# Performance work log

Measured on AMD Instinct MI355X. Metric: run time of the kernel, lower is better.

Reference implementation:

```python
import jax, jax.numpy as jnp
import numpy as np

B, S, A = 4096, 512, 64  # batch, state_dim, n_actions
H1, H2 = 1024, 512       # hidden_dims
EPS = 1e-8


def setup_inputs() -> dict:
    key = jax.random.key(0)
    ks = jax.random.split(key, 7)
    return {
        "states": jax.random.normal(ks[0], (B, S), dtype=jnp.float32),
        "W1": jax.random.normal(ks[1], (H1, S + A), dtype=jnp.float32) * 0.05,
        "b1": jax.random.normal(ks[2], (H1,), dtype=jnp.float32) * 0.01,
        "W2": jax.random.normal(ks[3], (H2, H1), dtype=jnp.float32) * 0.05,
        "b2": jax.random.normal(ks[4], (H2,), dtype=jnp.float32) * 0.01,
        "Wq": jax.random.normal(ks[5], (1, H2), dtype=jnp.float32) * 0.05,
        "bq": jax.random.normal(ks[6], (1,), dtype=jnp.float32) * 0.01,
    }


def _ff_layer(h, W, b):
    # L2-normalize over feature dim (torch dim=1 for 2D input), then linear + ReLU
    hn = h / (jnp.linalg.norm(h, axis=-1, keepdims=True) + EPS)
    return jax.nn.relu(jnp.einsum("abi,oi->abo", hn, W) + b)


def reference(states, W1, b1, W2, b2, Wq, bq):
    # Vectorized form of q_values: loop over actions becomes a leading axis a.
    # x_in[a, b] = concat(states[b], one_hot(a))  (overlay_type='standard')
    onehot = jnp.eye(A, dtype=states.dtype)                         # [A, A]
    x = jnp.concatenate(
        [jnp.broadcast_to(states[None], (A, B, S)),
         jnp.broadcast_to(onehot[:, None, :], (A, B, A))], axis=-1)  # [A, B, S+A]
    h = _ff_layer(x, W1, b1)   # [A, B, H1]
    h = _ff_layer(h, W2, b2)   # [A, B, H2]
    q = jnp.einsum("abh,oh->abo", h, Wq)[..., 0] + bq[0]            # [A, B]
    return q.T                                                       # [B, A]
```

## Files before the change

### kernel.cpp

```cpp
#include <hip/hip_runtime.h>
#include <stdint.h>

#define NB 4096
#define NS 512
#define NA 64
#define NH1 1024
#define NH2 512

typedef __attribute__((ext_vector_type(8))) short bf16x8;
typedef __attribute__((ext_vector_type(4))) float f32x4;

__device__ __forceinline__ unsigned short f2bf(float f) {
    union { float f; unsigned u; } v; v.f = f;
    return (unsigned short)((v.u + 0x8000u) >> 16);
}
__device__ __forceinline__ float bf2f(unsigned short h) {
    union { float f; unsigned u; } v; v.u = ((unsigned)h) << 16;
    return v.f;
}
__device__ __forceinline__ float bflo(unsigned u) {
    union { unsigned u; float f; } v; v.u = u << 16; return v.f;
}
__device__ __forceinline__ float bfhi(unsigned u) {
    union { unsigned u; float f; } v; v.u = u & 0xFFFF0000u; return v.f;
}
__device__ __forceinline__ unsigned packtrunc(float lo, float hi) {
    union { float f; unsigned u; } a, b; a.f = lo; b.f = hi;
    return __builtin_amdgcn_perm(b.u, a.u, 0x07060302u);
}
__device__ __forceinline__ void split2(float x, unsigned short& h, unsigned short& l) {
    unsigned short hh = f2bf(x);
    h = hh;
    l = f2bf(x - bf2f(hh));
}

__global__ void knorm(const float* __restrict__ S, float* __restrict__ nb) {
    int b = blockIdx.x; int l = threadIdx.x;
    const float* row = S + b * NS;
    float s = 0.f;
    for (int k = l; k < NS; k += 64) { float v = row[k]; s = fmaf(v, v, s); }
    for (int off = 32; off; off >>= 1) s += __shfl_down(s, off, 64);
    if (l == 0) nb[b] = sqrtf(s + 1.0f) + 1e-8f;
}

__global__ void kprep(const float* __restrict__ W1, const float* __restrict__ W2,
                      unsigned short* __restrict__ W2f, unsigned short* __restrict__ caT2,
                      unsigned short* __restrict__ W1hf, unsigned short* __restrict__ W1lf) {
    int i = blockIdx.x * 256 + threadIdx.x;
    if (i < 524288) {
        int j = i & 7; int l = (i >> 3) & 63; int c = (i >> 9) & 31; int kc = i >> 14;
        int n = c * 16 + (l >> 2);
        int g = (l & 3) ^ ((n >> 1) & 3);
        int k = kc * 32 + g * 8 + j;
        W2f[i] = f2bf(W2[(size_t)n * NH1 + k]);
    } else if (i < 589824) {
        int j2 = i - 524288;
        int kk = j2 & 31; int a_loc = (j2 >> 5) & 15;
        int kc = (j2 >> 9) & 31; int att = j2 >> 14;
        int o = kc * 32 + kk;
        caT2[j2] = f2bf(W1[(size_t)o * 576 + 512 + att * 16 + a_loc]);
    } else {
        int i2 = i - 589824;
        int kk = i2 & 31; int n = (i2 >> 5) & 1023; int kc = i2 >> 15;
        float x = W1[(size_t)n * 576 + kc * 32 + kk];
        unsigned short h, l;
        split2(x, h, l);
        W1hf[i2] = h;
        W1lf[i2] = l;
    }
}

__global__ __launch_bounds__(256) void kgemm1(
        const float* __restrict__ Sm,
        const unsigned short* __restrict__ W1hf, const unsigned short* __restrict__ W1lf,
        const float* __restrict__ b1, const float* __restrict__ nb,
        unsigned short* __restrict__ Gt) {
    const int m0 = (blockIdx.x >> 4) * 64;
    const int n0 = (blockIdx.x & 15) * 64;
    __shared__ unsigned short Ah[64][40], Al[64][40];
    int t = threadIdx.x;
    int lane = t & 63, wave = t >> 6;
    int wr = wave >> 1, wc = wave & 1;
    int qd = lane >> 4, cl = lane & 15;
    int r = t >> 2, seg = t & 3;
    f32x4 acc[2][2] = {};

    const unsigned short* gBh = W1hf + (size_t)(n0 + wc * 32 + cl) * 32 + qd * 8;
    const unsigned short* gBl = W1lf + (size_t)(n0 + wc * 32 + cl) * 32 + qd * 8;

    for (int k0 = 0; k0 < 512; k0 += 32) {
        {
            const float4* as4 = (const float4*)(Sm + (size_t)(m0 + r) * NS + k0 + seg * 8);
            unsigned* ah = (unsigned*)&Ah[r][seg * 8];
            unsigned* al = (unsigned*)&Al[r][seg * 8];
#pragma unroll
            for (int v = 0; v < 2; v++) {
                float4 fa = as4[v];
                unsigned short h0,h1,h2,h3,l0,l1,l2,l3;
                split2(fa.x,h0,l0); split2(fa.y,h1,l1); split2(fa.z,h2,l2); split2(fa.w,h3,l3);
                ah[v*2]   = (unsigned)h0 | ((unsigned)h1 << 16);
                ah[v*2+1] = (unsigned)h2 | ((unsigned)h3 << 16);
                al[v*2]   = (unsigned)l0 | ((unsigned)l1 << 16);
                al[v*2+1] = (unsigned)l2 | ((unsigned)l3 << 16);
            }
        }
        bf16x8 b_h[2], b_l[2];
#pragma unroll
        for (int nt = 0; nt < 2; nt++) {
            b_h[nt] = *(const bf16x8*)(gBh + nt * 512);
            b_l[nt] = *(const bf16x8*)(gBl + nt * 512);
        }
        gBh += 32768;
        gBl += 32768;
        __syncthreads();
        bf16x8 a_h[2], a_l[2];
#pragma unroll
        for (int mt = 0; mt < 2; mt++) {
            a_h[mt] = *(const bf16x8*)&Ah[wr*32 + mt*16 + cl][qd*8];
            a_l[mt] = *(const bf16x8*)&Al[wr*32 + mt*16 + cl][qd*8];
        }
#pragma unroll
        for (int mt = 0; mt < 2; mt++)
#pragma unroll
            for (int nt = 0; nt < 2; nt++) {
                acc[mt][nt] = __builtin_amdgcn_mfma_f32_16x16x32_bf16(a_h[mt], b_h[nt], acc[mt][nt], 0, 0, 0);
                acc[mt][nt] = __builtin_amdgcn_mfma_f32_16x16x32_bf16(a_h[mt], b_l[nt], acc[mt][nt], 0, 0, 0);
                acc[mt][nt] = __builtin_amdgcn_mfma_f32_16x16x32_bf16(a_l[mt], b_h[nt], acc[mt][nt], 0, 0, 0);
            }
        __syncthreads();
    }
#pragma unroll
    for (int mt = 0; mt < 2; mt++)
#pragma unroll
        for (int i = 0; i < 4; i++) {
            int m = m0 + wr*32 + mt*16 + qd*4 + i;
            float nbv = nb[m];
#pragma unroll
            for (int nt = 0; nt < 2; nt++) {
                int n = n0 + wc*32 + nt*16 + cl;
                float val = fmaf(b1[n], nbv, acc[mt][nt][i]);
                Gt[((size_t)(n >> 5) * NB + m) * 32 + (n & 31)] = f2bf(val);
            }
        }
}

__global__ __launch_bounds__(256, 2) void kmain(
        const unsigned short* __restrict__ Gt,
        const unsigned short* __restrict__ caT2,
        const unsigned short* __restrict__ W2f,
        const float* __restrict__ nb,
        const float* __restrict__ b2, const float* __restrict__ Wq,
        const float* __restrict__ bq, float* __restrict__ out) {
    int bid = blockIdx.x;
    int at = bid & 3;
    int bt = bid >> 2;

    __shared__ __align__(16) unsigned short As[8][64][40];
    __shared__ float invnh[64];
    __shared__ float qred[64][4];

    int t = threadIdx.x;
    int lane = t & 63, wc = t >> 6;
    int l15 = lane & 15, l4 = lane >> 4;

    int row = t >> 2, kd = t & 3;
    int ab = row >> 2, bb = row & 3;
    const unsigned short* gG = Gt + ((size_t)(bt * 4 + bb)) * 32 + kd * 8;
    const unsigned short* gC = caT2 + (size_t)at * 16384 + ab * 32 + kd * 8;

    float sq = 0.f;
    f32x4 acc[4][8] = {};
    bf16x8 g_v, c_v;

    auto agen = [&](int slot) {
        const unsigned* gd = (const unsigned*)&g_v;
        const unsigned* cd = (const unsigned*)&c_v;
        unsigned ow[4];
#pragma unroll
        for (int p = 0; p < 4; p++) {
            float u0 = fmaxf(bflo(gd[p]) + bflo(cd[p]), 0.f);
            float u1 = fmaxf(bfhi(gd[p]) + bfhi(cd[p]), 0.f);
            sq = fmaf(u0, u0, sq);
            sq = fmaf(u1, u1, sq);
            ow[p] = packtrunc(u0, u1);
        }
        *(bf16x8*)&As[slot][row][kd * 8] = *(bf16x8*)ow;
    };

    const int boff = (wc * 128 + l15) * 32 + ((l4 ^ ((l15 >> 1) & 3)) << 3);
    const unsigned short* gB = W2f + boff;

    bf16x8 bfrL[4], bfrH[4];

    g_v = *(const bf16x8*)gG;
    c_v = *(const bf16x8*)gC;
#pragma unroll
    for (int p = 0; p < 4; ++p) {
        agen(p);
        gG += (size_t)NB * 32;
        gC += 512;
        g_v = *(const bf16x8*)gG;
        c_v = *(const bf16x8*)gC;
    }
#pragma unroll
    for (int j = 0; j < 4; j++)
        bfrL[j] = *(const bf16x8*)(gB + j * 512);
#pragma unroll
    for (int j = 0; j < 4; j++)
        bfrH[j] = *(const bf16x8*)(gB + (4 + j) * 512);
    gB += 16384;

    for (int it = 0; it < 32; ++it) {
        if ((it & 3) == 0) {
            asm volatile("s_waitcnt lgkmcnt(0)" ::: "memory");
            __builtin_amdgcn_s_barrier();
            __builtin_amdgcn_sched_barrier(0);
        }
        int rs = it & 7;

        bf16x8 af[4];
#pragma unroll
        for (int mt = 0; mt < 4; mt++)
            af[mt] = *(const bf16x8*)&As[rs][mt * 16 + l15][l4 * 8];

        if (it < 28) agen((it + 4) & 7);
        if (it < 27) {
            gG += (size_t)NB * 32;
            gC += 512;
            g_v = *(const bf16x8*)gG;
            c_v = *(const bf16x8*)gC;
        }

        __builtin_amdgcn_s_setprio(1);
#pragma unroll
        for (int nt = 0; nt < 4; nt++)
#pragma unroll
            for (int mt = 0; mt < 4; mt++)
                acc[mt][nt] = __builtin_amdgcn_mfma_f32_16x16x32_bf16(af[mt], bfrL[nt], acc[mt][nt], 0, 0, 0);
        __builtin_amdgcn_s_setprio(0);

        if (it < 31) {
#pragma unroll
            for (int j = 0; j < 4; j++)
                bfrL[j] = *(const bf16x8*)(gB + j * 512);
        }

        __builtin_amdgcn_s_setprio(1);
#pragma unroll
        for (int nt = 0; nt < 4; nt++)
#pragma unroll
            for (int mt = 0; mt < 4; mt++)
                acc[mt][4 + nt] = __builtin_amdgcn_mfma_f32_16x16x32_bf16(af[mt], bfrH[nt], acc[mt][4 + nt], 0, 0, 0);
        __builtin_amdgcn_s_setprio(0);

        if (it < 31) {
#pragma unroll
            for (int j = 0; j < 4; j++)
                bfrH[j] = *(const bf16x8*)(gB + (4 + j) * 512);
            gB += 16384;
        }
    }

    sq += __shfl_xor(sq, 1, 64);
    sq += __shfl_xor(sq, 2, 64);
    if (kd == 0) invnh[row] = 1.0f / (sqrtf(sq) + 1e-8f * nb[bt * 4 + bb]);
    __syncthreads();

    float wqv[8], b2v[8];
#pragma unroll
    for (int nt = 0; nt < 8; nt++) {
        int o = wc * 128 + nt * 16 + l15;
        wqv[nt] = Wq[o]; b2v[nt] = b2[o];
    }
#pragma unroll
    for (int mt = 0; mt < 4; mt++) {
#pragma unroll
        for (int i = 0; i < 4; i++) {
            int R = mt * 16 + l4 * 4 + i;
            float inv = invnh[R];
            float qp = 0.f;
#pragma unroll
            for (int nt = 0; nt < 8; nt++) {
                float z = fmaf(acc[mt][nt][i], inv, b2v[nt]);
                z = fmaxf(z, 0.f);
                qp = fmaf(z, wqv[nt], qp);
            }
            qp += __shfl_xor(qp, 1, 64);
            qp += __shfl_xor(qp, 2, 64);
            qp += __shfl_xor(qp, 4, 64);
            qp += __shfl_xor(qp, 8, 64);
            if (l15 == 0) qred[R][wc] = qp;
        }
    }
    __syncthreads();
    if (t < 64) {
        float qv = qred[t][0] + qred[t][1] + qred[t][2] + qred[t][3] + bq[0];
        int aa = at * 16 + (t >> 2);
        int bo = bt * 4 + (t & 3);
        out[(size_t)bo * NA + aa] = qv;
    }
}

extern "C" void kernel_launch(void* const* d_in, const int* in_sizes, int n_in,
                              void* d_out, int out_size, void* d_ws, size_t ws_size,
                              hipStream_t stream) {
    const float* states = (const float*)d_in[0];
    const float* W1     = (const float*)d_in[1];
    const float* b1     = (const float*)d_in[2];
    const float* W2     = (const float*)d_in[3];
    const float* b2     = (const float*)d_in[4];
    const float* Wq     = (const float*)d_in[5];
    const float* bq     = (const float*)d_in[6];
    float* out = (float*)d_out;

    char* ws = (char*)d_ws;
    unsigned short* Gt   = (unsigned short*)ws;
    unsigned short* W2f  = (unsigned short*)(ws + (8u << 20));
    unsigned short* caT2 = (unsigned short*)(ws + (9u << 20));
    float*          nbp  = (float*)(ws + (9u << 20) + (128u << 10));
    unsigned short* W1hf = (unsigned short*)(ws + (9u << 20) + (256u << 10));
    unsigned short* W1lf = (unsigned short*)(ws + (10u << 20) + (256u << 10));

    knorm<<<NB, 64, 0, stream>>>(states, nbp);
    kprep<<<4352, 256, 0, stream>>>(W1, W2, W2f, caT2, W1hf, W1lf);
    kgemm1<<<1024, 256, 0, stream>>>(states, W1hf, W1lf, b1, nbp, Gt);
    kmain<<<4096, 256, 0, stream>>>(Gt, caT2, W2f, nbp, b2, Wq, bq, out);
}
```

Baseline: 314.8 us.

## Fuse row-norm computation into gemm1 and stagger kmain block starts

Removes the separate knorm kernel. kgemm1 now accumulates each state row's sum of squares while it loads and splits the tile, reduces across the four threads sharing a row, and keeps the norm in shared memory. The blocks with n0==0 also write it to global memory for kmain. Separately, kmain blocks sleep for a small hash-dependent delay at start to desynchronise their memory access. The delay adds idle cycles and its benefit is uncertain.

```diff
diff --git a/kernel.cpp b/kernel.cpp
--- a/kernel.cpp
+++ b/kernel.cpp
@@ -32,15 +32,6 @@
     unsigned short hh = f2bf(x);
     h = hh;
     l = f2bf(x - bf2f(hh));
-}
-
-__global__ void knorm(const float* __restrict__ S, float* __restrict__ nb) {
-    int b = blockIdx.x; int l = threadIdx.x;
-    const float* row = S + b * NS;
-    float s = 0.f;
-    for (int k = l; k < NS; k += 64) { float v = row[k]; s = fmaf(v, v, s); }
-    for (int off = 32; off; off >>= 1) s += __shfl_down(s, off, 64);
-    if (l == 0) nb[b] = sqrtf(s + 1.0f) + 1e-8f;
 }
 
 __global__ void kprep(const float* __restrict__ W1, const float* __restrict__ W2,
@@ -73,17 +64,19 @@
 __global__ __launch_bounds__(256) void kgemm1(
         const float* __restrict__ Sm,
         const unsigned short* __restrict__ W1hf, const unsigned short* __restrict__ W1lf,
-        const float* __restrict__ b1, const float* __restrict__ nb,
+        const float* __restrict__ b1, float* __restrict__ nb,
         unsigned short* __restrict__ Gt) {
     const int m0 = (blockIdx.x >> 4) * 64;
     const int n0 = (blockIdx.x & 15) * 64;
     __shared__ unsigned short Ah[64][40], Al[64][40];
+    __shared__ float nbl[64];
     int t = threadIdx.x;
     int lane = t & 63, wave = t >> 6;
     int wr = wave >> 1, wc = wave & 1;
     int qd = lane >> 4, cl = lane & 15;
     int r = t >> 2, seg = t & 3;
     f32x4 acc[2][2] = {};
+    float sqa = 0.f;
 
     const unsigned short* gBh = W1hf + (size_t)(n0 + wc * 32 + cl) * 32 + qd * 8;
     const unsigned short* gBl = W1lf + (size_t)(n0 + wc * 32 + cl) * 32 + qd * 8;
@@ -96,6 +89,10 @@
 #pragma unroll
             for (int v = 0; v < 2; v++) {
                 float4 fa = as4[v];
+                sqa = fmaf(fa.x, fa.x, sqa);
+                sqa = fmaf(fa.y, fa.y, sqa);
+                sqa = fmaf(fa.z, fa.z, sqa);
+                sqa = fmaf(fa.w, fa.w, sqa);
                 unsigned short h0,h1,h2,h3,l0,l1,l2,l3;
                 split2(fa.x,h0,l0); split2(fa.y,h1,l1); split2(fa.z,h2,l2); split2(fa.w,h3,l3);
                 ah[v*2]   = (unsigned)h0 | ((unsigned)h1 << 16);
@@ -129,16 +126,26 @@
             }
         __syncthreads();
     }
+
+    sqa += __shfl_xor(sqa, 1, 64);
+    sqa += __shfl_xor(sqa, 2, 64);
+    float nbv = sqrtf(sqa + 1.0f) + 1e-8f;
+    if ((t & 3) == 0) {
+        nbl[r] = nbv;
+        if (n0 == 0) nb[m0 + r] = nbv;
+    }
+    __syncthreads();
+
 #pragma unroll
     for (int mt = 0; mt < 2; mt++)
 #pragma unroll
         for (int i = 0; i < 4; i++) {
             int m = m0 + wr*32 + mt*16 + qd*4 + i;
-            float nbv = nb[m];
+            float nbm = nbl[wr*32 + mt*16 + qd*4 + i];
 #pragma unroll
             for (int nt = 0; nt < 2; nt++) {
                 int n = n0 + wc*32 + nt*16 + cl;
-                float val = fmaf(b1[n], nbv, acc[mt][nt][i]);
+                float val = fmaf(b1[n], nbm, acc[mt][nt][i]);
                 Gt[((size_t)(n >> 5) * NB + m) * 32 + (n & 31)] = f2bf(val);
             }
         }
@@ -154,6 +161,12 @@
     int bid = blockIdx.x;
     int at = bid & 3;
     int bt = bid >> 2;
+
+    {
+        unsigned lvl = ((unsigned)bid * 0x9E3779B9u) >> 30;
+        if (lvl & 1) __builtin_amdgcn_s_sleep(5);
+        if (lvl & 2) { __builtin_amdgcn_s_sleep(5); __builtin_amdgcn_s_sleep(5); }
+    }
 
     __shared__ __align__(16) unsigned short As[8][64][40];
     __shared__ float invnh[64];
@@ -321,7 +334,6 @@
     unsigned short* W1hf = (unsigned short*)(ws + (9u << 20) + (256u << 10));
     unsigned short* W1lf = (unsigned short*)(ws + (10u << 20) + (256u << 10));
 
-    knorm<<<NB, 64, 0, stream>>>(states, nbp);
     kprep<<<4352, 256, 0, stream>>>(W1, W2, W2f, caT2, W1hf, W1lf);
     kgemm1<<<1024, 256, 0, stream>>>(states, W1hf, W1lf, b1, nbp, Gt);
     kmain<<<4096, 256, 0, stream>>>(Gt, caT2, W2f, nbp, b2, Wq, bq, out);
```

New measurement: 314.4 us. About the same (-0.1%).
